# Optimization experiments

Measured on AMD Instinct MI355X. Metric: run time of the kernel, lower is better.

## Reference

```python
import jax, jax.numpy as jnp
import numpy as np

B, T, D_MODEL, D_HEAD = 8, 2048, 1024, 64


def setup_inputs() -> dict:
    key = jax.random.key(0)
    kx, kq, kk, kv = jax.random.split(key, 4)
    s = 1.0 / np.sqrt(D_MODEL)
    return {
        "x": jax.random.normal(kx, (B, T, D_MODEL), dtype=jnp.float32),
        "W_Q": jax.random.normal(kq, (D_MODEL, D_HEAD), dtype=jnp.float32) * s,
        "W_K": jax.random.normal(kk, (D_MODEL, D_HEAD), dtype=jnp.float32) * s,
        "W_V": jax.random.normal(kv, (D_MODEL, D_HEAD), dtype=jnp.float32) * s,
    }


def reference(x, W_Q, W_K, W_V):
    # x: [B, T, d_model]; projections -> [B, T, d_head]
    q = jnp.einsum("btd,dh->bth", x, W_Q)
    k = jnp.einsum("btd,dh->bth", x, W_K)
    v = jnp.einsum("btd,dh->bth", x, W_V)
    d_head = W_Q.shape[-1]
    scale = 1.0 / jnp.sqrt(jnp.asarray(d_head, dtype=x.dtype))
    # scores: [B, T, T], causal mask (lower-triangular kept)
    scores = jnp.einsum("bqh,bkh->bqk", q, k) * scale
    T_ = x.shape[1]
    causal = jnp.tril(jnp.ones((T_, T_), dtype=bool))
    scores = jnp.where(causal[None, :, :], scores, jnp.asarray(-jnp.inf, dtype=x.dtype))
    a = jax.nn.softmax(scores, axis=-1)
    # dropout omitted (eval mode / identity)
    out = jnp.einsum("bqk,bkh->bqh", a, v)
    return out
```

## Files before the change

### kernel.cpp

```cpp
#include <hip/hip_runtime.h>

#define TT   2048
#define DM   1024
#define DH   64
#define NB   8
#define KST  72
#define VST  264

typedef __attribute__((ext_vector_type(4))) float          f32x4;
typedef __attribute__((ext_vector_type(4))) int            i32x4;
typedef __attribute__((ext_vector_type(4))) unsigned short u16x4;
typedef __attribute__((ext_vector_type(8))) short          s16x8;

__device__ __forceinline__ unsigned short f2bf(float f) {
  unsigned int u = __float_as_uint(f);
  u += 0x7fffu + ((u >> 16) & 1u);
  return (unsigned short)(u >> 16);
}

#define MFMA(acc, a, b) \
  (acc) = __builtin_amdgcn_mfma_f32_16x16x32_bf16((a), (b), (acc), 0, 0, 0)

__device__ __forceinline__ void gload_lds16(const void* g, void* l) {
  __builtin_amdgcn_global_load_lds(
      (const __attribute__((address_space(1))) void*)g,
      (__attribute__((address_space(3))) void*)l, 16, 0, 0);
}

#define WS_WT    0u
#define WS_QK    393216u
#define WS_VT    4587520u
#define WS_OP    6684672u
#define WS_ML    16121856u

__global__ __launch_bounds__(256) void pack_w_kernel(
    const float* __restrict__ wq, const float* __restrict__ wk,
    const float* __restrict__ wv, unsigned short* __restrict__ wt) {
  int idx = blockIdx.x * 256 + threadIdx.x;
  if (idx >= 192 * DM) return;
  int n = idx >> 10;
  int k = idx & (DM - 1);
  const float* src = (n < 64) ? wq : ((n < 128) ? wk : wv);
  wt[(size_t)n * DM + k] = f2bf(src[(size_t)k * DH + (n & 63)]);
}

__global__ __launch_bounds__(256) void qkv_gemm_kernel(
    const float* __restrict__ x, const unsigned short* __restrict__ wt,
    unsigned short* __restrict__ qkvqk, unsigned short* __restrict__ vt) {
  __shared__ __align__(16) float          a_lds[32 * 64];
  __shared__ __align__(16) unsigned short b_lds[192 * 64];

  const int tid  = threadIdx.x;
  const int lane = tid & 63;
  const int w    = tid >> 6;
  const int ln   = lane & 15;
  const int quad = lane >> 4;
  const int mw   = w & 1;
  const int nw   = w >> 1;
  const int m0   = blockIdx.x * 32;
  const int n0   = nw * 96;
  const int lsw  = ln & 7;

  int agoff[2];
  #pragma unroll
  for (int i = 0; i < 2; ++i) {
    int s = i * 256 + w * 64 + lane;
    int m = s >> 4, cc = s & 15;
    agoff[i] = (m0 + m) * DM + ((cc ^ (m & 7)) << 2);
  }
  int bgoff[6];
  #pragma unroll
  for (int j = 0; j < 6; ++j) {
    int s = j * 256 + w * 64 + lane;
    int n = s >> 3, cc = s & 7;
    bgoff[j] = n * DM + ((cc ^ (n & 7)) << 3);
  }

  f32x4 acc[6];
  #pragma unroll
  for (int i = 0; i < 6; ++i) acc[i] = (f32x4){0.f, 0.f, 0.f, 0.f};
  union { s16x8 v; unsigned short h[8]; } ap;

  #pragma unroll
  for (int i = 0; i < 2; ++i)
    gload_lds16(x + agoff[i], (void*)(a_lds + (i * 256 + w * 64) * 4));
  #pragma unroll
  for (int j = 0; j < 6; ++j)
    gload_lds16(wt + bgoff[j], (void*)(b_lds + (j * 256 + w * 64) * 8));

  for (int k0 = 0; k0 < DM; k0 += 64) {
    __syncthreads();
    #pragma unroll
    for (int ks = 0; ks < 64; ks += 32) {
      const int m  = mw * 16 + ln;
      const int c0 = (ks >> 2) + 2 * quad;
      f32x4 v0 = *(const f32x4*)&a_lds[m * 64 + ((c0 ^ lsw) << 2)];
      f32x4 v1 = *(const f32x4*)&a_lds[m * 64 + (((c0 + 1) ^ lsw) << 2)];
      #pragma unroll
      for (int j = 0; j < 4; ++j) { ap.h[j] = f2bf(v0[j]); ap.h[4 + j] = f2bf(v1[j]); }
      s16x8 af = ap.v;
      const int cb = (ks >> 3) + quad;
      #pragma unroll
      for (int nt = 0; nt < 6; ++nt) {
        int n = n0 + nt * 16 + ln;
        s16x8 bf = *(const s16x8*)&b_lds[n * 64 + ((cb ^ lsw) << 3)];
        MFMA(acc[nt], af, bf);
      }
    }
    __syncthreads();
    if (k0 + 64 < DM) {
      const int kn = k0 + 64;
      #pragma unroll
      for (int i = 0; i < 2; ++i)
        gload_lds16(x + agoff[i] + kn, (void*)(a_lds + (i * 256 + w * 64) * 4));
      #pragma unroll
      for (int j = 0; j < 6; ++j)
        gload_lds16(wt + bgoff[j] + kn, (void*)(b_lds + (j * 256 + w * 64) * 8));
    }
  }

  const float QS = 0.18033688011112042f;
  const int mm0 = m0 + mw * 16;
  const int bz  = mm0 >> 11;
  const int tb  = (mm0 & 2047) + quad * 4;
  #pragma unroll
  for (int nt = 0; nt < 6; ++nt) {
    const int ncol = n0 + nt * 16 + ln;
    if (ncol < 128) {
      const float sc = (ncol < 64) ? QS : 1.0f;
      #pragma unroll
      for (int r = 0; r < 4; ++r) {
        int row = mm0 + quad * 4 + r;
        qkvqk[(size_t)row * 128 + ncol] = f2bf(acc[nt][r] * sc);
      }
    } else {
      int d = ncol - 128;
      u16x4 h;
      #pragma unroll
      for (int r = 0; r < 4; ++r) h[r] = f2bf(acc[nt][r]);
      *(u16x4*)(vt + ((size_t)bz * 64 + d) * TT + tb) = h;
    }
  }
}

__global__ __launch_bounds__(256) void attn_part_kernel(
    const unsigned short* __restrict__ qkvqk, const unsigned short* __restrict__ vt,
    unsigned short* __restrict__ opart, float* __restrict__ ml) {
  const int c  = blockIdx.x;
  const int qt = blockIdx.y;
  const int bz = blockIdx.z;
  const int aq = qt >> 2, rq = qt & 3;
  if (c > aq) return;
  const int ntiles = (c == aq) ? (rq + 1) : 4;

  __shared__ __align__(16) unsigned short k_lds[256 * KST];
  __shared__ __align__(16) unsigned short v_lds[64 * VST];
  __shared__ __align__(16) unsigned short p_lds[64 * KST];

  const int tid  = threadIdx.x;
  const int w    = tid >> 6;
  const int lane = tid & 63;
  const int ln   = lane & 15;
  const int quad = lane >> 4;
  const int bb   = bz * TT;
  const int kbase = c * 256;

  #pragma unroll
  for (int i = 0; i < 8; ++i) {
    int cid = i * 256 + tid;
    int row = cid >> 3, dc = (cid & 7) * 8;
    *(i32x4*)&k_lds[row * KST + dc] =
        *(const i32x4*)(qkvqk + (size_t)(bb + kbase + row) * 128 + 64 + dc);
  }
  #pragma unroll
  for (int i = 0; i < 8; ++i) {
    int cid = i * 256 + tid;
    int d = cid >> 5, tc = (cid & 31) * 8;
    *(i32x4*)&v_lds[d * VST + tc] =
        *(const i32x4*)(vt + ((size_t)bz * 64 + d) * TT + kbase + tc);
  }

  const unsigned short* qrow = qkvqk + (size_t)(bb + qt * 64 + w * 16 + ln) * 128;
  const s16x8 qf0 = *(const s16x8*)(qrow + quad * 8);
  const s16x8 qf1 = *(const s16x8*)(qrow + 32 + quad * 8);

  s16x8 ones;
  #pragma unroll
  for (int j = 0; j < 8; ++j) ones[j] = (short)0x3F80;

  f32x4 acc_o[4], acc_l;
  #pragma unroll
  for (int i = 0; i < 4; ++i) acc_o[i] = (f32x4){0.f, 0.f, 0.f, 0.f};
  acc_l = (f32x4){0.f, 0.f, 0.f, 0.f};

  const int qg_base = qt * 64 + w * 16 + quad * 4;
  __syncthreads();

  for (int ct = 0; ct < ntiles; ++ct) {
    const int ktg = c * 4 + ct;
    const bool diag = (ktg == qt);

    f32x4 acc_s[4];
    #pragma unroll
    for (int i = 0; i < 4; ++i) acc_s[i] = (f32x4){0.f, 0.f, 0.f, 0.f};
    #pragma unroll
    for (int ns = 0; ns < 4; ++ns) {
      s16x8 kf0 = *(const s16x8*)&k_lds[(ct * 64 + ns * 16 + ln) * KST + quad * 8];
      s16x8 kf1 = *(const s16x8*)&k_lds[(ct * 64 + ns * 16 + ln) * KST + 32 + quad * 8];
      MFMA(acc_s[ns], qf0, kf0);
      MFMA(acc_s[ns], qf1, kf1);
    }

    #pragma unroll
    for (int r = 0; r < 4; ++r) {
      const int qg = qg_base + r;
      #pragma unroll
      for (int ns = 0; ns < 4; ++ns) {
        float s = acc_s[ns][r];
        if (diag) {
          int kg = ktg * 64 + ns * 16 + ln;
          s = (kg <= qg) ? s : -1e30f;
        }
        float p = exp2f(s);
        p_lds[(w * 16 + quad * 4 + r) * KST + ns * 16 + ln] = f2bf(p);
      }
    }
    #pragma unroll
    for (int kk = 0; kk < 64; kk += 32) {
      s16x8 pf = *(const s16x8*)&p_lds[(w * 16 + ln) * KST + kk + quad * 8];
      MFMA(acc_l, pf, ones);
      #pragma unroll
      for (int nt = 0; nt < 4; ++nt) {
        s16x8 vf = *(const s16x8*)&v_lds[(nt * 16 + ln) * VST + ct * 64 + kk + quad * 8];
        MFMA(acc_o[nt], pf, vf);
      }
    }
    asm volatile("" ::: "memory");
  }

  const int base = qt + 2 * aq * (aq - 1) + rq * aq;
  const size_t slab = (size_t)bz * 144 + base + c;
  unsigned short* op = opart + slab * 4096;
  #pragma unroll
  for (int nt = 0; nt < 4; ++nt)
    #pragma unroll
    for (int r = 0; r < 4; ++r)
      op[(w * 16 + quad * 4 + r) * 64 + nt * 16 + ln] = f2bf(acc_o[nt][r]);
  if (ln == 0) {
    float* lp = ml + slab * 64;
    #pragma unroll
    for (int r = 0; r < 4; ++r)
      lp[w * 16 + quad * 4 + r] = acc_l[r];
  }
}

__global__ __launch_bounds__(256) void attn_combine_kernel(
    const unsigned short* __restrict__ opart, const float* __restrict__ ml,
    float* __restrict__ out) {
  const int qt = blockIdx.x;
  const int bz = blockIdx.y;
  const int aq = qt >> 2, rq = qt & 3;
  const int nch = aq + 1;
  const int base = qt + 2 * aq * (aq - 1) + rq * aq;
  const size_t slab0 = (size_t)bz * 144 + base;

  const int tid = threadIdx.x;
  const int row = tid >> 2;
  const int ds  = (tid & 3) * 16;

  float L = 0.f;
  float acc[16];
  #pragma unroll
  for (int j = 0; j < 16; ++j) acc[j] = 0.f;
  #pragma unroll 8
  for (int ch = 0; ch < nch; ++ch) {
    L += ml[(slab0 + ch) * 64 + row];
    const unsigned short* op = opart + (slab0 + ch) * 4096 + row * 64 + ds;
    i32x4 v0 = *(const i32x4*)(op);
    i32x4 v1 = *(const i32x4*)(op + 8);
    #pragma unroll
    for (int j = 0; j < 4; ++j) {
      unsigned int u0 = (unsigned int)v0[j], u1 = (unsigned int)v1[j];
      acc[j * 2]         += __uint_as_float(u0 << 16);
      acc[j * 2 + 1]     += __uint_as_float(u0 & 0xffff0000u);
      acc[8 + j * 2]     += __uint_as_float(u1 << 16);
      acc[8 + j * 2 + 1] += __uint_as_float(u1 & 0xffff0000u);
    }
  }
  float inv = 1.0f / L;
  float* o = out + ((size_t)bz * TT + qt * 64 + row) * 64 + ds;
  #pragma unroll
  for (int j = 0; j < 16; ++j) o[j] = acc[j] * inv;
}

extern "C" void kernel_launch(void* const* d_in, const int* in_sizes, int n_in,
                              void* d_out, int out_size, void* d_ws, size_t ws_size,
                              hipStream_t stream) {
  const float* x  = (const float*)d_in[0];
  const float* wq = (const float*)d_in[1];
  const float* wk = (const float*)d_in[2];
  const float* wv = (const float*)d_in[3];
  float* out = (float*)d_out;

  char* ws = (char*)d_ws;
  unsigned short* wt    = (unsigned short*)(ws + WS_WT);
  unsigned short* qkvqk = (unsigned short*)(ws + WS_QK);
  unsigned short* vt    = (unsigned short*)(ws + WS_VT);
  unsigned short* opart = (unsigned short*)(ws + WS_OP);
  float*          ml    = (float*)(ws + WS_ML);

  pack_w_kernel<<<(192 * DM + 255) / 256, 256, 0, stream>>>(wq, wk, wv, wt);
  qkv_gemm_kernel<<<NB * TT / 32, 256, 0, stream>>>(x, wt, qkvqk, vt);
  attn_part_kernel<<<dim3(8, 32, NB), 256, 0, stream>>>(qkvqk, vt, opart, ml);
  attn_combine_kernel<<<dim3(32, NB), 256, 0, stream>>>(opart, ml, out);
}
```

Measured before the change: 146.9 us.

## Fuse combine into attention partial kernel via atomic last-block reduction

Removes the separate combine kernel. The last partial-attention block to finish for each query tile, detected with an atomic counter, performs the reduction and writes the output. The grid is also compacted from a 3D launch with early-exit idle blocks to a 1D launch over only the valid (batch, tile, chunk) triples. This saves one kernel launch and the idle blocks, at the cost of threadfences, an atomic per block, and counters that are reset inside pack_w_kernel.

```diff
diff --git a/kernel.cpp b/kernel.cpp
--- a/kernel.cpp
+++ b/kernel.cpp
@@ -32,11 +32,14 @@
 #define WS_VT    4587520u
 #define WS_OP    6684672u
 #define WS_ML    16121856u
+#define WS_CNT   16416768u
 
 __global__ __launch_bounds__(256) void pack_w_kernel(
     const float* __restrict__ wq, const float* __restrict__ wk,
-    const float* __restrict__ wv, unsigned short* __restrict__ wt) {
+    const float* __restrict__ wv, unsigned short* __restrict__ wt,
+    int* __restrict__ cnt) {
   int idx = blockIdx.x * 256 + threadIdx.x;
+  if (blockIdx.x == 0 && threadIdx.x < NB * 32) cnt[threadIdx.x] = 0;
   if (idx >= 192 * DM) return;
   int n = idx >> 10;
   int k = idx & (DM - 1);
@@ -145,17 +148,26 @@
 
 __global__ __launch_bounds__(256) void attn_part_kernel(
     const unsigned short* __restrict__ qkvqk, const unsigned short* __restrict__ vt,
-    unsigned short* __restrict__ opart, float* __restrict__ ml) {
-  const int c  = blockIdx.x;
-  const int qt = blockIdx.y;
-  const int bz = blockIdx.z;
-  const int aq = qt >> 2, rq = qt & 3;
-  if (c > aq) return;
-  const int ntiles = (c == aq) ? (rq + 1) : 4;
+    unsigned short* __restrict__ opart, float* __restrict__ ml,
+    int* __restrict__ cnt, float* __restrict__ out) {
+  const int f  = blockIdx.x;
+  const int bz = f / 144;
+  const int rw = f - bz * 144;
+  int g = 0;
+  #pragma unroll
+  for (int t = 1; t < 8; ++t) if (rw >= 2 * t * (t + 1)) g = t;
+  const int rr = rw - 2 * g * (g + 1);
+  const int dq = rr / (g + 1);
+  const int qt = 4 * g + dq;
+  const int c  = rr - dq * (g + 1);
+  const int rq = qt & 3;
+  const int ntiles = (c == g) ? (rq + 1) : 4;
+  const int nch    = g + 1;
 
   __shared__ __align__(16) unsigned short k_lds[256 * KST];
   __shared__ __align__(16) unsigned short v_lds[64 * VST];
   __shared__ __align__(16) unsigned short p_lds[64 * KST];
+  __shared__ int is_last;
 
   const int tid  = threadIdx.x;
   const int w    = tid >> 6;
@@ -238,36 +250,31 @@
     asm volatile("" ::: "memory");
   }
 
-  const int base = qt + 2 * aq * (aq - 1) + rq * aq;
-  const size_t slab = (size_t)bz * 144 + base + c;
-  unsigned short* op = opart + slab * 4096;
+  const int base = qt + 2 * g * (g - 1) + rq * g;
+  const size_t slab0 = (size_t)bz * 144 + base;
+  unsigned short* op = opart + (slab0 + c) * 4096;
   #pragma unroll
   for (int nt = 0; nt < 4; ++nt)
     #pragma unroll
     for (int r = 0; r < 4; ++r)
       op[(w * 16 + quad * 4 + r) * 64 + nt * 16 + ln] = f2bf(acc_o[nt][r]);
   if (ln == 0) {
-    float* lp = ml + slab * 64;
+    float* lp = ml + (slab0 + c) * 64;
     #pragma unroll
     for (int r = 0; r < 4; ++r)
       lp[w * 16 + quad * 4 + r] = acc_l[r];
   }
-}
-
-__global__ __launch_bounds__(256) void attn_combine_kernel(
-    const unsigned short* __restrict__ opart, const float* __restrict__ ml,
-    float* __restrict__ out) {
-  const int qt = blockIdx.x;
-  const int bz = blockIdx.y;
-  const int aq = qt >> 2, rq = qt & 3;
-  const int nch = aq + 1;
-  const int base = qt + 2 * aq * (aq - 1) + rq * aq;
-  const size_t slab0 = (size_t)bz * 144 + base;
-
-  const int tid = threadIdx.x;
+
+  __threadfence();
+  __syncthreads();
+  if (tid == 0)
+    is_last = (atomicAdd(&cnt[bz * 32 + qt], 1) == nch - 1);
+  __syncthreads();
+  if (!is_last) return;
+  __threadfence();
+
   const int row = tid >> 2;
   const int ds  = (tid & 3) * 16;
-
   float L = 0.f;
   float acc[16];
   #pragma unroll
@@ -275,9 +282,9 @@
   #pragma unroll 8
   for (int ch = 0; ch < nch; ++ch) {
     L += ml[(slab0 + ch) * 64 + row];
-    const unsigned short* op = opart + (slab0 + ch) * 4096 + row * 64 + ds;
-    i32x4 v0 = *(const i32x4*)(op);
-    i32x4 v1 = *(const i32x4*)(op + 8);
+    const unsigned short* opc = opart + (slab0 + ch) * 4096 + row * 64 + ds;
+    i32x4 v0 = *(const i32x4*)(opc);
+    i32x4 v1 = *(const i32x4*)(opc + 8);
     #pragma unroll
     for (int j = 0; j < 4; ++j) {
       unsigned int u0 = (unsigned int)v0[j], u1 = (unsigned int)v1[j];
@@ -308,9 +315,9 @@
   unsigned short* vt    = (unsigned short*)(ws + WS_VT);
   unsigned short* opart = (unsigned short*)(ws + WS_OP);
   float*          ml    = (float*)(ws + WS_ML);
-
-  pack_w_kernel<<<(192 * DM + 255) / 256, 256, 0, stream>>>(wq, wk, wv, wt);
+  int*            cnt   = (int*)(ws + WS_CNT);
+
+  pack_w_kernel<<<(192 * DM + 255) / 256, 256, 0, stream>>>(wq, wk, wv, wt, cnt);
   qkv_gemm_kernel<<<NB * TT / 32, 256, 0, stream>>>(x, wt, qkvqk, vt);
-  attn_part_kernel<<<dim3(8, 32, NB), 256, 0, stream>>>(qkvqk, vt, opart, ml);
-  attn_combine_kernel<<<dim3(32, NB), 256, 0, stream>>>(opart, ml, out);
-}
+  attn_part_kernel<<<NB * 144, 256, 0, stream>>>(qkvqk, vt, opart, ml, cnt, out);
+}
```

New measurement: 362.8 us. 147% more time.

## Process two query tiles per block to reuse staged K/V and compact grid

Applied to the files above, without the earlier changes.

Each attention-part block now handles a pair of adjacent 64-row query tiles against the same 256-key chunk, so the K and V tiles staged in LDS are reused for both. The grid becomes a flat list of only the valid (pair, chunk) work items via a lookup table, which removes the early-exit blocks of the old 3D grid. The K/V load loops shrink to only the tiles actually needed. In exchange, per-block register use rises from the doubled accumulators, there are fewer blocks to fill the device, and the two halves run one after another through a shared P buffer.

```diff
diff --git a/kernel.cpp b/kernel.cpp
--- a/kernel.cpp
+++ b/kernel.cpp
@@ -146,12 +146,16 @@
 __global__ __launch_bounds__(256) void attn_part_kernel(
     const unsigned short* __restrict__ qkvqk, const unsigned short* __restrict__ vt,
     unsigned short* __restrict__ opart, float* __restrict__ ml) {
-  const int c  = blockIdx.x;
-  const int qt = blockIdx.y;
-  const int bz = blockIdx.z;
-  const int aq = qt >> 2, rq = qt & 3;
-  if (c > aq) return;
-  const int ntiles = (c == aq) ? (rq + 1) : 4;
+  const int Ctab[16] = {0,1,2,4,6,9,12,16,20,25,30,36,42,49,56,64};
+  const int f  = blockIdx.x;
+  const int bz = f / 72;
+  const int rw = f - bz * 72;
+  int s = 0;
+  #pragma unroll
+  for (int t = 1; t < 16; ++t) if (rw >= Ctab[t]) s = t;
+  const int c = rw - Ctab[s];
+  const int ntiles = min(4, 2 * s + 2 - 4 * c);
+  const int qtA = 2 * s, qtB = 2 * s + 1;
 
   __shared__ __align__(16) unsigned short k_lds[256 * KST];
   __shared__ __align__(16) unsigned short v_lds[64 * VST];
@@ -165,92 +169,145 @@
   const int bb   = bz * TT;
   const int kbase = c * 256;
 
-  #pragma unroll
-  for (int i = 0; i < 8; ++i) {
+  for (int i = 0; i < 2 * ntiles; ++i) {
     int cid = i * 256 + tid;
     int row = cid >> 3, dc = (cid & 7) * 8;
     *(i32x4*)&k_lds[row * KST + dc] =
         *(const i32x4*)(qkvqk + (size_t)(bb + kbase + row) * 128 + 64 + dc);
   }
-  #pragma unroll
-  for (int i = 0; i < 8; ++i) {
+  const int cm = ntiles * 8 - 1;
+  const int dshift = (ntiles == 4) ? 5 : 4;
+  for (int i = 0; i < 2 * ntiles; ++i) {
     int cid = i * 256 + tid;
-    int d = cid >> 5, tc = (cid & 31) * 8;
+    int d = cid >> dshift, tc = (cid & cm) * 8;
     *(i32x4*)&v_lds[d * VST + tc] =
         *(const i32x4*)(vt + ((size_t)bz * 64 + d) * TT + kbase + tc);
   }
 
-  const unsigned short* qrow = qkvqk + (size_t)(bb + qt * 64 + w * 16 + ln) * 128;
-  const s16x8 qf0 = *(const s16x8*)(qrow + quad * 8);
-  const s16x8 qf1 = *(const s16x8*)(qrow + 32 + quad * 8);
+  const unsigned short* qrowA = qkvqk + (size_t)(bb + qtA * 64 + w * 16 + ln) * 128;
+  const unsigned short* qrowB = qrowA + 64 * 128;
+  const s16x8 qfA0 = *(const s16x8*)(qrowA + quad * 8);
+  const s16x8 qfA1 = *(const s16x8*)(qrowA + 32 + quad * 8);
+  const s16x8 qfB0 = *(const s16x8*)(qrowB + quad * 8);
+  const s16x8 qfB1 = *(const s16x8*)(qrowB + 32 + quad * 8);
 
   s16x8 ones;
   #pragma unroll
   for (int j = 0; j < 8; ++j) ones[j] = (short)0x3F80;
 
-  f32x4 acc_o[4], acc_l;
-  #pragma unroll
-  for (int i = 0; i < 4; ++i) acc_o[i] = (f32x4){0.f, 0.f, 0.f, 0.f};
-  acc_l = (f32x4){0.f, 0.f, 0.f, 0.f};
-
-  const int qg_base = qt * 64 + w * 16 + quad * 4;
+  f32x4 acc_oA[4], acc_oB[4], acc_lA, acc_lB;
+  #pragma unroll
+  for (int i = 0; i < 4; ++i) {
+    acc_oA[i] = (f32x4){0.f, 0.f, 0.f, 0.f};
+    acc_oB[i] = (f32x4){0.f, 0.f, 0.f, 0.f};
+  }
+  acc_lA = (f32x4){0.f, 0.f, 0.f, 0.f};
+  acc_lB = (f32x4){0.f, 0.f, 0.f, 0.f};
+
+  const int qgA = qtA * 64 + w * 16 + quad * 4;
+  const int qgB = qgA + 64;
   __syncthreads();
 
   for (int ct = 0; ct < ntiles; ++ct) {
     const int ktg = c * 4 + ct;
-    const bool diag = (ktg == qt);
-
-    f32x4 acc_s[4];
+
+    if (ktg <= qtA) {
+      const bool diag = (ktg == qtA);
+      f32x4 acc_s[4];
+      #pragma unroll
+      for (int i = 0; i < 4; ++i) acc_s[i] = (f32x4){0.f, 0.f, 0.f, 0.f};
+      #pragma unroll
+      for (int ns = 0; ns < 4; ++ns) {
+        s16x8 kf0 = *(const s16x8*)&k_lds[(ct * 64 + ns * 16 + ln) * KST + quad * 8];
+        s16x8 kf1 = *(const s16x8*)&k_lds[(ct * 64 + ns * 16 + ln) * KST + 32 + quad * 8];
+        MFMA(acc_s[ns], qfA0, kf0);
+        MFMA(acc_s[ns], qfA1, kf1);
+      }
+      #pragma unroll
+      for (int r = 0; r < 4; ++r) {
+        const int qg = qgA + r;
+        #pragma unroll
+        for (int ns = 0; ns < 4; ++ns) {
+          float sv = acc_s[ns][r];
+          if (diag) {
+            int kg = ktg * 64 + ns * 16 + ln;
+            sv = (kg <= qg) ? sv : -1e30f;
+          }
+          p_lds[(w * 16 + quad * 4 + r) * KST + ns * 16 + ln] = f2bf(exp2f(sv));
+        }
+      }
+      #pragma unroll
+      for (int kk = 0; kk < 64; kk += 32) {
+        s16x8 pf = *(const s16x8*)&p_lds[(w * 16 + ln) * KST + kk + quad * 8];
+        MFMA(acc_lA, pf, ones);
+        #pragma unroll
+        for (int nt = 0; nt < 4; ++nt) {
+          s16x8 vf = *(const s16x8*)&v_lds[(nt * 16 + ln) * VST + ct * 64 + kk + quad * 8];
+          MFMA(acc_oA[nt], pf, vf);
+        }
+      }
+      asm volatile("" ::: "memory");
+    }
+
+    {
+      const bool diag = (ktg == qtB);
+      f32x4 acc_s[4];
+      #pragma unroll
+      for (int i = 0; i < 4; ++i) acc_s[i] = (f32x4){0.f, 0.f, 0.f, 0.f};
+      #pragma unroll
+      for (int ns = 0; ns < 4; ++ns) {
+        s16x8 kf0 = *(const s16x8*)&k_lds[(ct * 64 + ns * 16 + ln) * KST + quad * 8];
+        s16x8 kf1 = *(const s16x8*)&k_lds[(ct * 64 + ns * 16 + ln) * KST + 32 + quad * 8];
+        MFMA(acc_s[ns], qfB0, kf0);
+        MFMA(acc_s[ns], qfB1, kf1);
+      }
+      #pragma unroll
+      for (int r = 0; r < 4; ++r) {
+        const int qg = qgB + r;
+        #pragma unroll
+        for (int ns = 0; ns < 4; ++ns) {
+          float sv = acc_s[ns][r];
+          if (diag) {
+            int kg = ktg * 64 + ns * 16 + ln;
+            sv = (kg <= qg) ? sv : -1e30f;
+          }
+          p_lds[(w * 16 + quad * 4 + r) * KST + ns * 16 + ln] = f2bf(exp2f(sv));
+        }
+      }
+      #pragma unroll
+      for (int kk = 0; kk < 64; kk += 32) {
+        s16x8 pf = *(const s16x8*)&p_lds[(w * 16 + ln) * KST + kk + quad * 8];
+        MFMA(acc_lB, pf, ones);
+        #pragma unroll
+        for (int nt = 0; nt < 4; ++nt) {
+          s16x8 vf = *(const s16x8*)&v_lds[(nt * 16 + ln) * VST + ct * 64 + kk + quad * 8];
+          MFMA(acc_oB[nt], pf, vf);
+        }
+      }
+      asm volatile("" ::: "memory");
+    }
+  }
+
+  #pragma unroll
+  for (int half = 0; half < 2; ++half) {
+    const int qt = (half == 0) ? qtA : qtB;
+    const int g  = qt >> 2, rq = qt & 3;
+    const int base = qt + 2 * g * (g - 1) + rq * g;
+    const size_t slab = (size_t)bz * 144 + base + c;
+    unsigned short* op = opart + slab * 4096;
+    const f32x4* ao = (half == 0) ? acc_oA : acc_oB;
+    const f32x4  al = (half == 0) ? acc_lA : acc_lB;
     #pragma unroll
-    for (int i = 0; i < 4; ++i) acc_s[i] = (f32x4){0.f, 0.f, 0.f, 0.f};
-    #pragma unroll
-    for (int ns = 0; ns < 4; ++ns) {
-      s16x8 kf0 = *(const s16x8*)&k_lds[(ct * 64 + ns * 16 + ln) * KST + quad * 8];
-      s16x8 kf1 = *(const s16x8*)&k_lds[(ct * 64 + ns * 16 + ln) * KST + 32 + quad * 8];
-      MFMA(acc_s[ns], qf0, kf0);
-      MFMA(acc_s[ns], qf1, kf1);
-    }
-
-    #pragma unroll
-    for (int r = 0; r < 4; ++r) {
-      const int qg = qg_base + r;
-      #pragma unroll
-      for (int ns = 0; ns < 4; ++ns) {
-        float s = acc_s[ns][r];
-        if (diag) {
-          int kg = ktg * 64 + ns * 16 + ln;
-          s = (kg <= qg) ? s : -1e30f;
-        }
-        float p = exp2f(s);
-        p_lds[(w * 16 + quad * 4 + r) * KST + ns * 16 + ln] = f2bf(p);
-      }
-    }
-    #pragma unroll
-    for (int kk = 0; kk < 64; kk += 32) {
-      s16x8 pf = *(const s16x8*)&p_lds[(w * 16 + ln) * KST + kk + quad * 8];
-      MFMA(acc_l, pf, ones);
-      #pragma unroll
-      for (int nt = 0; nt < 4; ++nt) {
-        s16x8 vf = *(const s16x8*)&v_lds[(nt * 16 + ln) * VST + ct * 64 + kk + quad * 8];
-        MFMA(acc_o[nt], pf, vf);
-      }
-    }
-    asm volatile("" ::: "memory");
-  }
-
-  const int base = qt + 2 * aq * (aq - 1) + rq * aq;
-  const size_t slab = (size_t)bz * 144 + base + c;
-  unsigned short* op = opart + slab * 4096;
-  #pragma unroll
-  for (int nt = 0; nt < 4; ++nt)
-    #pragma unroll
-    for (int r = 0; r < 4; ++r)
-      op[(w * 16 + quad * 4 + r) * 64 + nt * 16 + ln] = f2bf(acc_o[nt][r]);
-  if (ln == 0) {
-    float* lp = ml + slab * 64;
-    #pragma unroll
-    for (int r = 0; r < 4; ++r)
-      lp[w * 16 + quad * 4 + r] = acc_l[r];
+    for (int nt = 0; nt < 4; ++nt)
+      #pragma unroll
+      for (int r = 0; r < 4; ++r)
+        op[(w * 16 + quad * 4 + r) * 64 + nt * 16 + ln] = f2bf(ao[nt][r]);
+    if (ln == 0) {
+      float* lp = ml + slab * 64;
+      #pragma unroll
+      for (int r = 0; r < 4; ++r)
+        lp[w * 16 + quad * 4 + r] = al[r];
+    }
   }
 }
 
@@ -311,6 +368,6 @@
 
   pack_w_kernel<<<(192 * DM + 255) / 256, 256, 0, stream>>>(wq, wk, wv, wt);
   qkv_gemm_kernel<<<NB * TT / 32, 256, 0, stream>>>(x, wt, qkvqk, vt);
-  attn_part_kernel<<<dim3(8, 32, NB), 256, 0, stream>>>(qkvqk, vt, opart, ml);
+  attn_part_kernel<<<NB * 72, 256, 0, stream>>>(qkvqk, vt, opart, ml);
   attn_combine_kernel<<<dim3(32, NB), 256, 0, stream>>>(opart, ml, out);
 }
```

Measured after the change: 144.4 us. About the same (-1.7%).
